# Performance work log

Measured on AMD Instinct MI355X. Metric: run time of the kernel, lower is better.

Reference implementation:

```python
import jax, jax.numpy as jnp
import numpy as np

B, S, D, E, K = 2, 2048, 1024, 8, 2
H = 4 * D  # FFN hidden


def setup_inputs() -> dict:
    key = jax.random.key(0)
    ks = jax.random.split(key, 6)
    x = jax.random.normal(ks[0], (B, S, D), dtype=jnp.float32)
    # xavier-uniform gate
    lim_g = np.sqrt(6.0 / (D + E)).astype(np.float32)
    W_gate = jax.random.uniform(ks[1], (D, E), minval=-lim_g, maxval=lim_g, dtype=jnp.float32)
    # per-expert FFN params, stacked on leading expert axis
    lim1 = np.sqrt(1.0 / D).astype(np.float32)
    lim2 = np.sqrt(1.0 / H).astype(np.float32)
    W1 = jax.random.uniform(ks[2], (E, D, H), minval=-lim1, maxval=lim1, dtype=jnp.float32)
    b1 = jax.random.uniform(ks[3], (E, H), minval=-lim1, maxval=lim1, dtype=jnp.float32)
    W2 = jax.random.uniform(ks[4], (E, H, D), minval=-lim2, maxval=lim2, dtype=jnp.float32)
    b2 = jax.random.uniform(ks[5], (E, D), minval=-lim2, maxval=lim2, dtype=jnp.float32)
    return {"x": x, "W_gate": W_gate, "W1": W1, "b1": b1, "W2": W2, "b2": b2}


def reference(x, W_gate, W1, b1, W2, b2):
    # gating: topk mask then softmax over kept logits
    gate = jnp.einsum('bsd,de->bse', x, W_gate)                      # [B,S,E]
    kth = jax.lax.top_k(gate, K)[0][..., -1:]                        # k-th largest [B,S,1]
    mask = jax.nn.softmax(jnp.where(gate >= kth, gate, -jnp.inf), axis=-1)
    # all-experts FFN (faithful to original dense compute)
    h = jax.nn.relu(jnp.einsum('bsd,edh->bseh', x, W1) + b1)         # [B,S,E,H]
    y = jnp.einsum('bseh,ehd->bsed', h, W2) + b2                     # [B,S,E,D]
    # masked MEAN over experts (original uses .mean, i.e. divides by E)
    return (y * mask[..., None]).mean(axis=-2)                       # [B,S,D]
```

## Files before the change

### kernel.cpp

```cpp
#include <hip/hip_runtime.h>
#include <stdint.h>
#include <stddef.h>

#define TOK   4096
#define DDIM  1024
#define EXP   8
#define HDIM  4096

typedef __bf16 bf16x8 __attribute__((ext_vector_type(8)));
typedef __bf16 bf16x4 __attribute__((ext_vector_type(4)));
typedef float  f32x4  __attribute__((ext_vector_type(4)));

#define OFF_COUNTS 0ull
#define OFF_PREFIX 256ull
#define OFF_PERM   512ull
#define OFF_WGT    (OFF_PERM + 131072ull)
#define OFF_XBF    (OFF_WGT + 131072ull)
#define OFF_W1T    (OFF_XBF + 8388608ull)
#define OFF_W2T    (OFF_W1T + 67108864ull)
#define OFF_HBF    (OFF_W2T + 67108864ull)
#define OFF_T2E    (OFF_HBF + 68157440ull)

__device__ __forceinline__ void load16_lds(const void* g, void* l) {
  __builtin_amdgcn_global_load_lds((__attribute__((address_space(1))) void*)g,
                                   (__attribute__((address_space(3))) void*)l,
                                   16, 0, 0);
}

__global__ __launch_bounds__(256) void prep_kernel(
    const float* __restrict__ W1, const float* __restrict__ W2,
    __bf16* __restrict__ W1t, __bf16* __restrict__ W2t,
    const float* __restrict__ x, const float* __restrict__ Wg,
    __bf16* __restrict__ x_bf, int* __restrict__ counts,
    int* __restrict__ perm, float* __restrict__ wgt,
    int4* __restrict__ tok2exp)
{
  __shared__ float tile[64 * 65];
  const int bid = blockIdx.x;
  const int tid = threadIdx.x;

  if (bid < 64) {
    const int lane = tid & 63;
    const int wid  = tid >> 6;

    int*   lcnt   = (int*)tile;
    int*   gbase  = lcnt + 8;
    int*   rec_e  = gbase + 8;
    int*   rec_p  = rec_e + 64;
    float* rec_w0 = (float*)(rec_p + 64);
    float* rec_w1 = rec_w0 + 64;

    if (tid < 8) lcnt[tid] = 0;
    __syncthreads();

#pragma unroll 1
    for (int i = 0; i < 16; ++i) {
      const int li = wid * 16 + i;
      const int t  = bid * 64 + li;
      const float* xr = x + (size_t)t * DDIM;

      float acc[EXP];
#pragma unroll
      for (int e = 0; e < EXP; ++e) acc[e] = 0.f;

#pragma unroll
      for (int it = 0; it < 4; ++it) {
        const int d0 = it * 256 + lane * 4;
        float4 xv = *(const float4*)(xr + d0);
        bf16x4 xb = { (__bf16)xv.x, (__bf16)xv.y, (__bf16)xv.z, (__bf16)xv.w };
        *(bf16x4*)(x_bf + (size_t)t * DDIM + d0) = xb;
        const float* wrow = Wg + (size_t)d0 * EXP;
        float xs[4] = { xv.x, xv.y, xv.z, xv.w };
#pragma unroll
        for (int u = 0; u < 4; ++u) {
          float4 wa = *(const float4*)(wrow + u * 8);
          float4 wb = *(const float4*)(wrow + u * 8 + 4);
          acc[0] += xs[u] * wa.x; acc[1] += xs[u] * wa.y;
          acc[2] += xs[u] * wa.z; acc[3] += xs[u] * wa.w;
          acc[4] += xs[u] * wb.x; acc[5] += xs[u] * wb.y;
          acc[6] += xs[u] * wb.z; acc[7] += xs[u] * wb.w;
        }
      }
#pragma unroll
      for (int e = 0; e < EXP; ++e) {
        float v = acc[e];
#pragma unroll
        for (int s = 32; s > 0; s >>= 1) v += __shfl_down(v, s, 64);
        acc[e] = v;
      }
      if (lane == 0) {
        int e0 = 0; float g0 = acc[0];
#pragma unroll
        for (int e = 1; e < EXP; ++e) if (acc[e] > g0) { g0 = acc[e]; e0 = e; }
        int e1 = 0; float g1 = -3.4e38f;
#pragma unroll
        for (int e = 0; e < EXP; ++e) if (e != e0 && acc[e] > g1) { g1 = acc[e]; e1 = e; }
        float ex = __expf(g1 - g0);
        float m0 = 1.f / (1.f + ex);
        float m1 = ex  / (1.f + ex);
        int lp0 = atomicAdd(&lcnt[e0], 1);
        int lp1 = atomicAdd(&lcnt[e1], 1);
        rec_e[li]  = e0 | (e1 << 8);
        rec_p[li]  = lp0 | (lp1 << 16);
        rec_w0[li] = m0 * 0.125f;
        rec_w1[li] = m1 * 0.125f;
      }
    }
    __syncthreads();
    if (tid < 8) gbase[tid] = atomicAdd(&counts[tid], lcnt[tid]);
    __syncthreads();
    if (tid < 64) {
      const int t = bid * 64 + tid;
      const int ee = rec_e[tid], pp = rec_p[tid];
      const int e0 = ee & 0xff, e1 = ee >> 8;
      const int p0 = gbase[e0] + (pp & 0xffff);
      const int p1 = gbase[e1] + (pp >> 16);
      perm[e0 * TOK + p0] = t;  wgt[e0 * TOK + p0] = rec_w0[tid];
      perm[e1 * TOK + p1] = t;  wgt[e1 * TOK + p1] = rec_w1[tid];
      tok2exp[t] = make_int4(e0, p0, e1, p1);
    }
    return;
  }

  const int tb    = bid - 64;
  const int which = tb >> 13;
  const int e     = (tb >> 10) & 7;
  const int t10   = tb & 1023;
  const float* src; __bf16* dst; int Kd, Nd, tk, tn;
  if (which == 0) { Kd = 1024; Nd = 4096; src = W1; dst = W1t; tk = t10 & 15; tn = t10 >> 4; }
  else            { Kd = 4096; Nd = 1024; src = W2; dst = W2t; tk = t10 >> 4; tn = t10 & 15; }
  const int k0 = tk * 64, n0 = tn * 64;
  src += ((size_t)e * Kd + k0) * Nd + n0;
  dst += ((size_t)e * Nd + n0) * Kd + k0;

  const int lr = tid >> 4, lc = (tid & 15) * 4;
#pragma unroll
  for (int p = 0; p < 4; ++p) {
    const int r = p * 16 + lr;
    float4 v = *(const float4*)(src + (size_t)r * Nd + lc);
    tile[r * 65 + lc + 0] = v.x;
    tile[r * 65 + lc + 1] = v.y;
    tile[r * 65 + lc + 2] = v.z;
    tile[r * 65 + lc + 3] = v.w;
  }
  __syncthreads();
  const int n = tid >> 2, kcb = (tid & 3) * 8;
#pragma unroll
  for (int h = 0; h < 2; ++h) {
    const int kb = kcb + h * 32;
    bf16x8 o;
#pragma unroll
    for (int u = 0; u < 8; ++u) o[u] = (__bf16)tile[(kb + u) * 65 + n];
    *(bf16x8*)(dst + (size_t)n * Kd + kb) = o;
  }
}

__global__ void prefix_kernel(const int* __restrict__ counts, int* __restrict__ prefix)
{
  if (threadIdx.x == 0 && blockIdx.x == 0) {
    int s = 0;
    for (int e = 0; e < EXP; ++e) { prefix[e] = s; s += counts[e]; }
    prefix[EXP] = s;
  }
}

__global__ __launch_bounds__(256, 2) void gemm1_kernel(
    const __bf16* __restrict__ x_bf, const __bf16* __restrict__ W1t,
    const float* __restrict__ b1, __bf16* __restrict__ h_bf,
    const int* __restrict__ perm, const int* __restrict__ counts,
    const int* __restrict__ prefix)
{
  const int bid = blockIdx.x;
  const int e   = bid >> 10;
  const int mt  = (bid >> 5) & 31;
  const int nt  = bid & 31;
  const int cnt = counts[e];
  if (mt * 128 >= cnt) return;
  const int pfx = prefix[e];

  __shared__ __align__(16) __bf16 As[4096];
  __shared__ __align__(16) __bf16 Bs[4096];

  const int tid  = threadIdx.x;
  const int lane = tid & 63, wid = tid >> 6;
  const int wm = wid & 1, wn = wid >> 1;
  const int qd = lane >> 4, l15 = lane & 15;

  const int rA0 = tid >> 2, rA1 = rA0 + 64;
  const int pA0 = (tid & 3) ^ ((rA0 >> 1) & 3);
  const int pA1 = (tid & 3) ^ ((rA1 >> 1) & 3);
  int mA0 = mt * 128 + rA0; if (mA0 >= cnt) mA0 = cnt - 1;
  int mA1 = mt * 128 + rA1; if (mA1 >= cnt) mA1 = cnt - 1;
  const int tok0 = perm[e * TOK + mA0];
  const int tok1 = perm[e * TOK + mA1];
  const __bf16* gA0 = x_bf + (size_t)tok0 * DDIM + pA0 * 8;
  const __bf16* gA1 = x_bf + (size_t)tok1 * DDIM + pA1 * 8;
  const __bf16* Wte = W1t + (size_t)e * HDIM * DDIM;
  const __bf16* gB0 = Wte + (size_t)(nt * 128 + rA0) * DDIM + pA0 * 8;
  const __bf16* gB1 = Wte + (size_t)(nt * 128 + rA1) * DDIM + pA1 * 8;
  __bf16* ldsA0 = &As[tid * 8];
  __bf16* ldsA1 = &As[(tid + 256) * 8];
  __bf16* ldsB0 = &Bs[tid * 8];
  __bf16* ldsB1 = &Bs[(tid + 256) * 8];

  f32x4 acc[4][4] = {};

  for (int kk = 0; kk < DDIM; kk += 32) {
    __syncthreads();
    load16_lds(gA0 + kk, ldsA0);
    load16_lds(gA1 + kk, ldsA1);
    load16_lds(gB0 + kk, ldsB0);
    load16_lds(gB1 + kk, ldsB1);
    __syncthreads();
    bf16x8 af[4], bfr[4];
#pragma unroll
    for (int i = 0; i < 4; ++i) {
      int r = wm * 64 + i * 16 + l15;
      int ch = r * 4 + (qd ^ ((r >> 1) & 3));
      af[i] = *(const bf16x8*)(As + ch * 8);
    }
#pragma unroll
    for (int j = 0; j < 4; ++j) {
      int r = wn * 64 + j * 16 + l15;
      int ch = r * 4 + (qd ^ ((r >> 1) & 3));
      bfr[j] = *(const bf16x8*)(Bs + ch * 8);
    }
#pragma unroll
    for (int i = 0; i < 4; ++i)
#pragma unroll
      for (int j = 0; j < 4; ++j)
        acc[i][j] = __builtin_amdgcn_mfma_f32_16x16x32_bf16(af[i], bfr[j], acc[i][j], 0, 0, 0);
  }

  const float* b1e = b1 + (size_t)e * HDIM;
#pragma unroll
  for (int i = 0; i < 4; ++i) {
#pragma unroll
    for (int v = 0; v < 4; ++v) {
      const int rl = wm * 64 + i * 16 + qd * 4 + v;
      const int m  = mt * 128 + rl;
      if (m < cnt) {
        __bf16* hrow = h_bf + (size_t)(pfx + m) * HDIM;
#pragma unroll
        for (int j = 0; j < 4; ++j) {
          const int col = nt * 128 + wn * 64 + j * 16 + l15;
          float hv = acc[i][j][v] + b1e[col];
          hv = fmaxf(hv, 0.f);
          hrow[col] = (__bf16)hv;
        }
      }
    }
  }
}

__global__ __launch_bounds__(256, 2) void gemm2_kernel(
    const __bf16* __restrict__ h_bf, const __bf16* __restrict__ W2t,
    __bf16* __restrict__ Y,
    const int* __restrict__ counts, const int* __restrict__ prefix)
{
  const int bid = blockIdx.x;
  const int ks  = bid & 3;
  const int nt  = (bid >> 2) & 7;
  const int mt  = (bid >> 5) & 31;
  const int e   = bid >> 10;
  const int cnt = counts[e];
  if (mt * 128 >= cnt) return;
  const int pfx = prefix[e];

  __shared__ __align__(16) __bf16 As[4096];
  __shared__ __align__(16) __bf16 Bs[4096];

  const int tid  = threadIdx.x;
  const int lane = tid & 63, wid = tid >> 6;
  const int wm = wid & 1, wn = wid >> 1;
  const int qd = lane >> 4, l15 = lane & 15;

  const int rA0 = tid >> 2, rA1 = rA0 + 64;
  const int pA0 = (tid & 3) ^ ((rA0 >> 1) & 3);
  const int pA1 = (tid & 3) ^ ((rA1 >> 1) & 3);
  const __bf16* gA0 = h_bf + (size_t)(pfx + mt * 128 + rA0) * HDIM + pA0 * 8;
  const __bf16* gA1 = h_bf + (size_t)(pfx + mt * 128 + rA1) * HDIM + pA1 * 8;
  const __bf16* Wte = W2t + (size_t)e * DDIM * HDIM;
  const __bf16* gB0 = Wte + (size_t)(nt * 128 + rA0) * HDIM + pA0 * 8;
  const __bf16* gB1 = Wte + (size_t)(nt * 128 + rA1) * HDIM + pA1 * 8;
  __bf16* ldsA0 = &As[tid * 8];
  __bf16* ldsA1 = &As[(tid + 256) * 8];
  __bf16* ldsB0 = &Bs[tid * 8];
  __bf16* ldsB1 = &Bs[(tid + 256) * 8];

  f32x4 acc[4][4] = {};

  const int kbeg = ks * (HDIM / 4);
  const int kend = kbeg + (HDIM / 4);
  for (int kk = kbeg; kk < kend; kk += 32) {
    __syncthreads();
    load16_lds(gA0 + kk, ldsA0);
    load16_lds(gA1 + kk, ldsA1);
    load16_lds(gB0 + kk, ldsB0);
    load16_lds(gB1 + kk, ldsB1);
    __syncthreads();
    bf16x8 af[4], bfr[4];
#pragma unroll
    for (int i = 0; i < 4; ++i) {
      int r = wm * 64 + i * 16 + l15;
      int ch = r * 4 + (qd ^ ((r >> 1) & 3));
      af[i] = *(const bf16x8*)(As + ch * 8);
    }
#pragma unroll
    for (int j = 0; j < 4; ++j) {
      int r = wn * 64 + j * 16 + l15;
      int ch = r * 4 + (qd ^ ((r >> 1) & 3));
      bfr[j] = *(const bf16x8*)(Bs + ch * 8);
    }
#pragma unroll
    for (int i = 0; i < 4; ++i)
#pragma unroll
      for (int j = 0; j < 4; ++j)
        acc[i][j] = __builtin_amdgcn_mfma_f32_16x16x32_bf16(af[i], bfr[j], acc[i][j], 0, 0, 0);
  }

  __bf16* Ys = Y + (size_t)ks * (2 * TOK) * DDIM;
#pragma unroll
  for (int i = 0; i < 4; ++i) {
#pragma unroll
    for (int v = 0; v < 4; ++v) {
      const int rl = wm * 64 + i * 16 + qd * 4 + v;
      const int m  = mt * 128 + rl;
      if (m < cnt) {
        __bf16* yrow = Ys + (size_t)(pfx + m) * DDIM;
#pragma unroll
        for (int j = 0; j < 4; ++j) {
          const int col = nt * 128 + wn * 64 + j * 16 + l15;
          yrow[col] = (__bf16)acc[i][j][v];
        }
      }
    }
  }
}

__global__ __launch_bounds__(256) void combine_kernel(
    const __bf16* __restrict__ Y, const float* __restrict__ b2,
    const float* __restrict__ wgt, const int4* __restrict__ tok2exp,
    const int* __restrict__ prefix, float* __restrict__ out)
{
  const int t = blockIdx.x;
  const int c = threadIdx.x * 4;
  const int4 m = tok2exp[t];
  const int g0 = prefix[m.x] + m.y;
  const int g1 = prefix[m.z] + m.w;
  const float w0 = wgt[m.x * TOK + m.y];
  const float w1 = wgt[m.z * TOK + m.w];
  const size_t slab = (size_t)(2 * TOK) * DDIM;

  float s0x = 0.f, s0y = 0.f, s0z = 0.f, s0w = 0.f;
  float s1x = 0.f, s1y = 0.f, s1z = 0.f, s1w = 0.f;
#pragma unroll
  for (int s = 0; s < 4; ++s) {
    bf16x4 a = *(const bf16x4*)(Y + s * slab + (size_t)g0 * DDIM + c);
    bf16x4 b = *(const bf16x4*)(Y + s * slab + (size_t)g1 * DDIM + c);
    s0x += (float)a[0]; s0y += (float)a[1]; s0z += (float)a[2]; s0w += (float)a[3];
    s1x += (float)b[0]; s1y += (float)b[1]; s1z += (float)b[2]; s1w += (float)b[3];
  }
  float4 be0 = *(const float4*)(b2 + (size_t)m.x * DDIM + c);
  float4 be1 = *(const float4*)(b2 + (size_t)m.z * DDIM + c);
  float4 r;
  r.x = w0 * (s0x + be0.x) + w1 * (s1x + be1.x);
  r.y = w0 * (s0y + be0.y) + w1 * (s1y + be1.y);
  r.z = w0 * (s0z + be0.z) + w1 * (s1z + be1.z);
  r.w = w0 * (s0w + be0.w) + w1 * (s1w + be1.w);
  *(float4*)(out + (size_t)t * DDIM + c) = r;
}

extern "C" void kernel_launch(void* const* d_in, const int* in_sizes, int n_in,
                              void* d_out, int out_size, void* d_ws, size_t ws_size,
                              hipStream_t stream)
{
  const float* x  = (const float*)d_in[0];
  const float* Wg = (const float*)d_in[1];
  const float* W1 = (const float*)d_in[2];
  const float* b1 = (const float*)d_in[3];
  const float* W2 = (const float*)d_in[4];
  const float* b2 = (const float*)d_in[5];
  float* out = (float*)d_out;

  char* ws = (char*)d_ws;
  int*    counts  = (int*)(ws + OFF_COUNTS);
  int*    prefix  = (int*)(ws + OFF_PREFIX);
  int*    perm    = (int*)(ws + OFF_PERM);
  float*  wgt     = (float*)(ws + OFF_WGT);
  __bf16* x_bf    = (__bf16*)(ws + OFF_XBF);
  __bf16* W1t     = (__bf16*)(ws + OFF_W1T);
  __bf16* W2t     = (__bf16*)(ws + OFF_W2T);
  __bf16* h_bf    = (__bf16*)(ws + OFF_HBF);
  int4*   tok2exp = (int4*)(ws + OFF_T2E);
  __bf16* Y       = (__bf16*)(ws + OFF_W1T);

  hipMemsetAsync(counts, 0, 256, stream);

  prep_kernel<<<64 + 16384, 256, 0, stream>>>(W1, W2, W1t, W2t,
                                              x, Wg, x_bf, counts, perm, wgt, tok2exp);
  prefix_kernel<<<1, 64, 0, stream>>>(counts, prefix);
  gemm1_kernel<<<EXP * 32 * 32, 256, 0, stream>>>(x_bf, W1t, b1, h_bf, perm, counts, prefix);
  gemm2_kernel<<<EXP * 32 * 8 * 4, 256, 0, stream>>>(h_bf, W2t, Y, counts, prefix);
  combine_kernel<<<TOK, 256, 0, stream>>>(Y, b2, wgt, tok2exp, prefix, out);
}
```

Before: 523.5 us.

## Double-buffer GEMM LDS tiles, swizzle bf16 transpose tile, drop prefix kernel

Both grouped GEMMs now double-buffer their LDS A/B tiles, issuing the next k-step's direct-to-LDS loads before the MFMAs on the current buffer, with one barrier per iteration instead of two. The weight transpose in prep converts to bf16 before writing to LDS, using an XOR-swizzled 128-byte-per-row layout so each thread reads 16-byte vectors instead of eight scalar floats. The single-thread prefix kernel is removed and each block recomputes its expert offset from counts. This doubles LDS per GEMM block, which may reduce occupancy, and adds a few redundant count loads per block.

```diff
diff --git a/kernel.cpp b/kernel.cpp
--- a/kernel.cpp
+++ b/kernel.cpp
@@ -9,6 +9,7 @@
 
 typedef __bf16 bf16x8 __attribute__((ext_vector_type(8)));
 typedef __bf16 bf16x4 __attribute__((ext_vector_type(4)));
+typedef __bf16 bf16x2 __attribute__((ext_vector_type(2)));
 typedef float  f32x4  __attribute__((ext_vector_type(4)));
 
 #define OFF_COUNTS 0ull
@@ -35,7 +36,7 @@
     int* __restrict__ perm, float* __restrict__ wgt,
     int4* __restrict__ tok2exp)
 {
-  __shared__ float tile[64 * 65];
+  __shared__ __align__(16) float tile[2112];
   const int bid = blockIdx.x;
   const int tid = threadIdx.x;
 
@@ -133,42 +134,38 @@
   src += ((size_t)e * Kd + k0) * Nd + n0;
   dst += ((size_t)e * Nd + n0) * Kd + k0;
 
-  const int lr = tid >> 4, lc = (tid & 15) * 4;
-#pragma unroll
-  for (int p = 0; p < 4; ++p) {
-    const int r = p * 16 + lr;
-    float4 v = *(const float4*)(src + (size_t)r * Nd + lc);
-    tile[r * 65 + lc + 0] = v.x;
-    tile[r * 65 + lc + 1] = v.y;
-    tile[r * 65 + lc + 2] = v.z;
-    tile[r * 65 + lc + 3] = v.w;
+  char* tb8 = (char*)tile;
+  const int lr2 = (tid >> 4) * 2;
+  const int lc  = (tid & 15) * 4;
+#pragma unroll
+  for (int p = 0; p < 2; ++p) {
+    const int r = p * 32 + lr2;
+    float4 va = *(const float4*)(src + (size_t)r * Nd + lc);
+    float4 vb = *(const float4*)(src + (size_t)(r + 1) * Nd + lc);
+    float a4[4] = { va.x, va.y, va.z, va.w };
+    float b4[4] = { vb.x, vb.y, vb.z, vb.w };
+#pragma unroll
+    for (int j = 0; j < 4; ++j) {
+      const int n = lc + j;
+      bf16x2 w = { (__bf16)a4[j], (__bf16)b4[j] };
+      *(bf16x2*)(tb8 + n * 128 + ((r * 2) ^ (((n >> 2) & 7) << 4))) = w;
+    }
   }
   __syncthreads();
-  const int n = tid >> 2, kcb = (tid & 3) * 8;
+  const int n2 = tid >> 2, cb = tid & 3;
+  const int sw = (n2 >> 2) & 7;
 #pragma unroll
   for (int h = 0; h < 2; ++h) {
-    const int kb = kcb + h * 32;
-    bf16x8 o;
-#pragma unroll
-    for (int u = 0; u < 8; ++u) o[u] = (__bf16)tile[(kb + u) * 65 + n];
-    *(bf16x8*)(dst + (size_t)n * Kd + kb) = o;
-  }
-}
-
-__global__ void prefix_kernel(const int* __restrict__ counts, int* __restrict__ prefix)
-{
-  if (threadIdx.x == 0 && blockIdx.x == 0) {
-    int s = 0;
-    for (int e = 0; e < EXP; ++e) { prefix[e] = s; s += counts[e]; }
-    prefix[EXP] = s;
+    const int c = cb + h * 4;
+    bf16x8 o = *(const bf16x8*)(tb8 + n2 * 128 + ((c ^ sw) << 4));
+    *(bf16x8*)(dst + (size_t)n2 * Kd + c * 8) = o;
   }
 }
 
 __global__ __launch_bounds__(256, 2) void gemm1_kernel(
     const __bf16* __restrict__ x_bf, const __bf16* __restrict__ W1t,
     const float* __restrict__ b1, __bf16* __restrict__ h_bf,
-    const int* __restrict__ perm, const int* __restrict__ counts,
-    const int* __restrict__ prefix)
+    const int* __restrict__ perm, const int* __restrict__ counts)
 {
   const int bid = blockIdx.x;
   const int e   = bid >> 10;
@@ -176,10 +173,12 @@
   const int nt  = bid & 31;
   const int cnt = counts[e];
   if (mt * 128 >= cnt) return;
-  const int pfx = prefix[e];
-
-  __shared__ __align__(16) __bf16 As[4096];
-  __shared__ __align__(16) __bf16 Bs[4096];
+  int pfx = 0;
+#pragma unroll
+  for (int i = 0; i < EXP; ++i) if (i < e) pfx += counts[i];
+
+  __shared__ __align__(16) __bf16 As[2][4096];
+  __shared__ __align__(16) __bf16 Bs[2][4096];
 
   const int tid  = threadIdx.x;
   const int lane = tid & 63, wid = tid >> 6;
@@ -198,39 +197,43 @@
   const __bf16* Wte = W1t + (size_t)e * HDIM * DDIM;
   const __bf16* gB0 = Wte + (size_t)(nt * 128 + rA0) * DDIM + pA0 * 8;
   const __bf16* gB1 = Wte + (size_t)(nt * 128 + rA1) * DDIM + pA1 * 8;
-  __bf16* ldsA0 = &As[tid * 8];
-  __bf16* ldsA1 = &As[(tid + 256) * 8];
-  __bf16* ldsB0 = &Bs[tid * 8];
-  __bf16* ldsB1 = &Bs[(tid + 256) * 8];
+
+#define STAGE1(buf, kk) do { \
+    load16_lds(gA0 + (kk), &As[buf][tid * 8]); \
+    load16_lds(gA1 + (kk), &As[buf][(tid + 256) * 8]); \
+    load16_lds(gB0 + (kk), &Bs[buf][tid * 8]); \
+    load16_lds(gB1 + (kk), &Bs[buf][(tid + 256) * 8]); \
+  } while (0)
 
   f32x4 acc[4][4] = {};
 
+  STAGE1(0, 0);
+  __syncthreads();
+  int cur = 0;
   for (int kk = 0; kk < DDIM; kk += 32) {
-    __syncthreads();
-    load16_lds(gA0 + kk, ldsA0);
-    load16_lds(gA1 + kk, ldsA1);
-    load16_lds(gB0 + kk, ldsB0);
-    load16_lds(gB1 + kk, ldsB1);
-    __syncthreads();
+    if (kk + 32 < DDIM) STAGE1(cur ^ 1, kk + 32);
     bf16x8 af[4], bfr[4];
 #pragma unroll
     for (int i = 0; i < 4; ++i) {
       int r = wm * 64 + i * 16 + l15;
       int ch = r * 4 + (qd ^ ((r >> 1) & 3));
-      af[i] = *(const bf16x8*)(As + ch * 8);
+      af[i] = *(const bf16x8*)(&As[cur][ch * 8]);
     }
 #pragma unroll
     for (int j = 0; j < 4; ++j) {
       int r = wn * 64 + j * 16 + l15;
       int ch = r * 4 + (qd ^ ((r >> 1) & 3));
-      bfr[j] = *(const bf16x8*)(Bs + ch * 8);
+      bfr[j] = *(const bf16x8*)(&Bs[cur][ch * 8]);
     }
 #pragma unroll
     for (int i = 0; i < 4; ++i)
 #pragma unroll
       for (int j = 0; j < 4; ++j)
         acc[i][j] = __builtin_amdgcn_mfma_f32_16x16x32_bf16(af[i], bfr[j], acc[i][j], 0, 0, 0);
-  }
+    __syncthreads();
+    cur ^= 1;
+  }
+#undef STAGE1
 
   const float* b1e = b1 + (size_t)e * HDIM;
 #pragma unroll
@@ -256,7 +259,7 @@
 __global__ __launch_bounds__(256, 2) void gemm2_kernel(
     const __bf16* __restrict__ h_bf, const __bf16* __restrict__ W2t,
     __bf16* __restrict__ Y,
-    const int* __restrict__ counts, const int* __restrict__ prefix)
+    const int* __restrict__ counts)
 {
   const int bid = blockIdx.x;
   const int ks  = bid & 3;
@@ -265,10 +268,12 @@
   const int e   = bid >> 10;
   const int cnt = counts[e];
   if (mt * 128 >= cnt) return;
-  const int pfx = prefix[e];
-
-  __shared__ __align__(16) __bf16 As[4096];
-  __shared__ __align__(16) __bf16 Bs[4096];
+  int pfx = 0;
+#pragma unroll
+  for (int i = 0; i < EXP; ++i) if (i < e) pfx += counts[i];
+
+  __shared__ __align__(16) __bf16 As[2][4096];
+  __shared__ __align__(16) __bf16 Bs[2][4096];
 
   const int tid  = threadIdx.x;
   const int lane = tid & 63, wid = tid >> 6;
@@ -283,41 +288,45 @@
   const __bf16* Wte = W2t + (size_t)e * DDIM * HDIM;
   const __bf16* gB0 = Wte + (size_t)(nt * 128 + rA0) * HDIM + pA0 * 8;
   const __bf16* gB1 = Wte + (size_t)(nt * 128 + rA1) * HDIM + pA1 * 8;
-  __bf16* ldsA0 = &As[tid * 8];
-  __bf16* ldsA1 = &As[(tid + 256) * 8];
-  __bf16* ldsB0 = &Bs[tid * 8];
-  __bf16* ldsB1 = &Bs[(tid + 256) * 8];
+
+#define STAGE2(buf, kk) do { \
+    load16_lds(gA0 + (kk), &As[buf][tid * 8]); \
+    load16_lds(gA1 + (kk), &As[buf][(tid + 256) * 8]); \
+    load16_lds(gB0 + (kk), &Bs[buf][tid * 8]); \
+    load16_lds(gB1 + (kk), &Bs[buf][(tid + 256) * 8]); \
+  } while (0)
 
   f32x4 acc[4][4] = {};
 
   const int kbeg = ks * (HDIM / 4);
   const int kend = kbeg + (HDIM / 4);
+  STAGE2(0, kbeg);
+  __syncthreads();
+  int cur = 0;
   for (int kk = kbeg; kk < kend; kk += 32) {
-    __syncthreads();
-    load16_lds(gA0 + kk, ldsA0);
-    load16_lds(gA1 + kk, ldsA1);
-    load16_lds(gB0 + kk, ldsB0);
-    load16_lds(gB1 + kk, ldsB1);
-    __syncthreads();
+    if (kk + 32 < kend) STAGE2(cur ^ 1, kk + 32);
     bf16x8 af[4], bfr[4];
 #pragma unroll
     for (int i = 0; i < 4; ++i) {
       int r = wm * 64 + i * 16 + l15;
       int ch = r * 4 + (qd ^ ((r >> 1) & 3));
-      af[i] = *(const bf16x8*)(As + ch * 8);
+      af[i] = *(const bf16x8*)(&As[cur][ch * 8]);
     }
 #pragma unroll
     for (int j = 0; j < 4; ++j) {
       int r = wn * 64 + j * 16 + l15;
       int ch = r * 4 + (qd ^ ((r >> 1) & 3));
-      bfr[j] = *(const bf16x8*)(Bs + ch * 8);
+      bfr[j] = *(const bf16x8*)(&Bs[cur][ch * 8]);
     }
 #pragma unroll
     for (int i = 0; i < 4; ++i)
 #pragma unroll
       for (int j = 0; j < 4; ++j)
         acc[i][j] = __builtin_amdgcn_mfma_f32_16x16x32_bf16(af[i], bfr[j], acc[i][j], 0, 0, 0);
-  }
+    __syncthreads();
+    cur ^= 1;
+  }
+#undef STAGE2
 
   __bf16* Ys = Y + (size_t)ks * (2 * TOK) * DDIM;
 #pragma unroll
@@ -341,13 +350,20 @@
 __global__ __launch_bounds__(256) void combine_kernel(
     const __bf16* __restrict__ Y, const float* __restrict__ b2,
     const float* __restrict__ wgt, const int4* __restrict__ tok2exp,
-    const int* __restrict__ prefix, float* __restrict__ out)
+    const int* __restrict__ counts, float* __restrict__ out)
 {
   const int t = blockIdx.x;
   const int c = threadIdx.x * 4;
   const int4 m = tok2exp[t];
-  const int g0 = prefix[m.x] + m.y;
-  const int g1 = prefix[m.z] + m.w;
+  int base0 = 0, base1 = 0;
+#pragma unroll
+  for (int i = 0; i < EXP; ++i) {
+    int cc = counts[i];
+    if (i < m.x) base0 += cc;
+    if (i < m.z) base1 += cc;
+  }
+  const int g0 = base0 + m.y;
+  const int g1 = base1 + m.w;
   const float w0 = wgt[m.x * TOK + m.y];
   const float w1 = wgt[m.z * TOK + m.w];
   const size_t slab = (size_t)(2 * TOK) * DDIM;
@@ -385,7 +401,6 @@
 
   char* ws = (char*)d_ws;
   int*    counts  = (int*)(ws + OFF_COUNTS);
-  int*    prefix  = (int*)(ws + OFF_PREFIX);
   int*    perm    = (int*)(ws + OFF_PERM);
   float*  wgt     = (float*)(ws + OFF_WGT);
   __bf16* x_bf    = (__bf16*)(ws + OFF_XBF);
@@ -399,8 +414,7 @@
 
   prep_kernel<<<64 + 16384, 256, 0, stream>>>(W1, W2, W1t, W2t,
                                               x, Wg, x_bf, counts, perm, wgt, tok2exp);
-  prefix_kernel<<<1, 64, 0, stream>>>(counts, prefix);
-  gemm1_kernel<<<EXP * 32 * 32, 256, 0, stream>>>(x_bf, W1t, b1, h_bf, perm, counts, prefix);
-  gemm2_kernel<<<EXP * 32 * 8 * 4, 256, 0, stream>>>(h_bf, W2t, Y, counts, prefix);
-  combine_kernel<<<TOK, 256, 0, stream>>>(Y, b2, wgt, tok2exp, prefix, out);
-}
+  gemm1_kernel<<<EXP * 32 * 32, 256, 0, stream>>>(x_bf, W1t, b1, h_bf, perm, counts);
+  gemm2_kernel<<<EXP * 32 * 8 * 4, 256, 0, stream>>>(h_bf, W2t, Y, counts);
+  combine_kernel<<<TOK, 256, 0, stream>>>(Y, b2, wgt, tok2exp, counts, out);
+}
```

After: 540.5 us. 3.2% more time.
